# Kernel tuning notes

Hardware: AMD Instinct MI355X
Metric: run time of the kernel (lower is better)

Reference implementation:

```python
import jax, jax.numpy as jnp
import numpy as np

V, D, H, L, MAXS = 32000, 768, 12, 6, 2048
HD = D // H  # 64
FF = 4 * D
B, S = 8, 1024
EPS = 1e-5


def _make_pe():
    pos = np.arange(MAXS, dtype=np.float32)[:, None]
    div = np.exp(np.arange(0, D, 2, dtype=np.float32) * (-np.log(10000.0) / D))
    pe = np.zeros((MAXS, D), dtype=np.float32)
    pe[:, 0::2] = np.sin(pos * div)
    pe[:, 1::2] = np.cos(pos * div)
    return jnp.asarray(pe)


def setup_inputs() -> dict:
    key = jax.random.key(0)
    ks = jax.random.split(key, 16)
    sc = 0.02
    return {
        "tokens": jax.random.randint(ks[0], (B, S), 0, V),
        "k_mask": jnp.ones((B, S), dtype=jnp.int32),
        "emb": jax.random.normal(ks[1], (V, D), jnp.float32) * sc,
        "pe": _make_pe(),
        "ln1_s": jnp.ones((L, D), jnp.float32),
        "ln1_b": jnp.zeros((L, D), jnp.float32),
        "wq": jax.random.normal(ks[2], (L, H, D, HD), jnp.float32) * sc,
        "wk": jax.random.normal(ks[3], (L, H, D, HD), jnp.float32) * sc,
        "wv": jax.random.normal(ks[4], (L, H, D, HD), jnp.float32) * sc,
        "wo": jax.random.normal(ks[5], (L, D, D), jnp.float32) * sc,
        "ln2_s": jnp.ones((L, D), jnp.float32),
        "ln2_b": jnp.zeros((L, D), jnp.float32),
        "w1": jax.random.normal(ks[6], (L, D, FF), jnp.float32) * sc,
        "b1": jnp.zeros((L, FF), jnp.float32),
        "w2": jax.random.normal(ks[7], (L, FF, D), jnp.float32) * sc,
        "b2": jnp.zeros((L, D), jnp.float32),
    }


def _ln(x, s, b):
    m = jnp.mean(x, axis=-1, keepdims=True)
    v = jnp.var(x, axis=-1, keepdims=True)
    return (x - m) * jax.lax.rsqrt(v + EPS) * s + b


def _forward(tokens, k_mask, emb, pe, ln1_s, ln1_b, wq, wk, wv, wo,
             ln2_s, ln2_b, w1, b1, w2, b2):
    x = emb[tokens] + pe[None, :tokens.shape[1], :]  # [B,S,D]
    mask = (k_mask != 0)[:, None, None, :]  # [B,1,1,S]
    for l in range(L):
        xn = _ln(x, ln1_s[l], ln1_b[l])
        q = jnp.einsum('bsd,hde->bhse', xn, wq[l])
        k = jnp.einsum('bsd,hde->bhse', xn, wk[l])
        v = jnp.einsum('bsd,hde->bhse', xn, wv[l])
        scores = jnp.einsum('bhse,bhte->bhst', q, k) / (HD ** 0.5)
        scores = jnp.where(mask, scores, -jnp.inf)
        attn = jax.nn.softmax(scores, axis=-1)
        o = jnp.einsum('bhst,bhte->bhse', attn, v)  # [B,H,S,HD]
        o = o.transpose(0, 2, 1, 3).reshape(x.shape)  # concat heads -> [B,S,D]
        x = x + o @ wo[l]
        xn = _ln(x, ln2_s[l], ln2_b[l])
        h = jax.nn.gelu(xn @ w1[l] + b1[l], approximate=False)
        x = x + h @ w2[l] + b2[l]
    return x


def reference(tokens, k_mask, emb, pe, ln1_s, ln1_b, wq, wk, wv, wo,
              ln2_s, ln2_b, w1, b1, w2, b2):
    return _forward(tokens, k_mask, emb, pe, ln1_s, ln1_b, wq, wk, wv, wo,
                    ln2_s, ln2_b, w1, b1, w2, b2)
```

## Files before the change

kernel.cpp:

```cpp
#include <hip/hip_runtime.h>
#include <math.h>

typedef unsigned short u16;
typedef unsigned int u32;
typedef __attribute__((ext_vector_type(8))) __bf16 bf16x8;
typedef __attribute__((ext_vector_type(4))) float f32x4;
typedef __attribute__((ext_vector_type(8))) unsigned short ushort8v;
typedef __attribute__((ext_vector_type(4))) float float4v;
typedef __attribute__((ext_vector_type(4))) unsigned short u16x4;

typedef const __attribute__((address_space(1))) void gvoid_t;
typedef __attribute__((address_space(3))) void lvoid_t;

#define MFMA(a, b, c) __builtin_amdgcn_mfma_f32_16x16x32_bf16((a), (b), (c), 0, 0, 0)

__device__ __forceinline__ u16 f2bf(float f) {
  __bf16 h = (__bf16)f;
  return __builtin_bit_cast(u16, h);
}

__device__ __forceinline__ void stage64(const u16* g, int ldg, u16* lds, int rows, int tid) {
  int w = tid >> 6, l = tid & 63;
  int lr = l >> 3;
  int cb = (l & 7) << 4;
  for (int it = 0; it < rows; it += 32) {
    int rbase = it + w * 8;
    int r = rbase + lr;
    int scb = cb ^ ((r & 7) << 4);
    const char* gp = (const char*)(g + (size_t)r * ldg) + scb;
    char* lp = (char*)lds + (size_t)rbase * 128;
    __builtin_amdgcn_global_load_lds((gvoid_t*)gp, (lvoid_t*)lp, 16, 0, 0);
  }
}

__device__ __forceinline__ bf16x8 ldsfrag(const u16* base, int row, int e0) {
  int boff = row * 128 + (((e0) << 1) ^ ((row & 7) << 4));
  return *(const bf16x8*)((const char*)base + boff);
}

__global__ void embed_kernel(const int* __restrict__ tok, const float* __restrict__ emb,
                             const float* __restrict__ pe, float* __restrict__ xf) {
  int row = blockIdx.x;
  int tid = threadIdx.x;
  int t = tok[row];
  int spos = row & 1023;
  float4v e = ((const float4v*)(emb + (size_t)t * 768))[tid];
  float4v p = ((const float4v*)(pe + (size_t)spos * 768))[tid];
  float4v r;
  r.x = e.x + p.x; r.y = e.y + p.y; r.z = e.z + p.z; r.w = e.w + p.w;
  ((float4v*)(xf + (size_t)row * 768))[tid] = r;
}

__global__ void ln_kernel(const float* __restrict__ x, const float* __restrict__ sc,
                          const float* __restrict__ bi, u16* __restrict__ out) {
  int row = blockIdx.x;
  int tid = threadIdx.x;
  float4v v = ((const float4v*)(x + (size_t)row * 768))[tid];
  float s = v.x + v.y + v.z + v.w;
  float s2 = v.x * v.x + v.y * v.y + v.z * v.z + v.w * v.w;
  #pragma unroll
  for (int off = 32; off >= 1; off >>= 1) {
    s += __shfl_down(s, off);
    s2 += __shfl_down(s2, off);
  }
  __shared__ float red[8];
  if ((tid & 63) == 0) { red[tid >> 6] = s; red[4 + (tid >> 6)] = s2; }
  __syncthreads();
  float S = red[0] + red[1] + red[2];
  float S2 = red[4] + red[5] + red[6];
  float m = S * (1.0f / 768.0f);
  float var = S2 * (1.0f / 768.0f) - m * m;
  float rs = rsqrtf(var + 1e-5f);
  float4v sv = ((const float4v*)sc)[tid];
  float4v bv = ((const float4v*)bi)[tid];
  u16x4 ov;
  ov.x = f2bf((v.x - m) * rs * sv.x + bv.x);
  ov.y = f2bf((v.y - m) * rs * sv.y + bv.y);
  ov.z = f2bf((v.z - m) * rs * sv.z + bv.z);
  ov.w = f2bf((v.w - m) * rs * sv.w + bv.w);
  *(u16x4*)(out + (size_t)row * 768 + tid * 4) = ov;
}

__global__ void convT_kernel(const float* __restrict__ src, u16* __restrict__ dst,
                             int N, int K, long long sz, long long dz) {
  src += (size_t)blockIdx.z * sz;
  dst += (size_t)blockIdx.z * dz;
  __shared__ float t[32][33];
  int n0 = blockIdx.x * 32, k0 = blockIdx.y * 32;
  int tid = threadIdx.x;
  int tx = tid & 31, ty = tid >> 5;
  for (int r = ty; r < 32; r += 8) t[r][tx] = src[(size_t)(k0 + r) * N + n0 + tx];
  __syncthreads();
  for (int r = ty; r < 32; r += 8) dst[(size_t)(n0 + r) * K + k0 + tx] = f2bf(t[tx][r]);
}

__global__ void convqkvT_kernel(const float* __restrict__ wq, const float* __restrict__ wk,
                                const float* __restrict__ wv, u16* __restrict__ dst,
                                long long wz, long long dz) {
  __shared__ float t[32][33];
  int n0 = blockIdx.x * 32, k0 = blockIdx.y * 32;
  int which = n0 / 768;
  int r0 = n0 % 768;
  int h = r0 >> 6, e0 = r0 & 63;
  const float* src = which == 0 ? wq : (which == 1 ? wk : wv);
  src += (size_t)blockIdx.z * wz;
  dst += (size_t)blockIdx.z * dz;
  int tid = threadIdx.x;
  int tx = tid & 31, ty = tid >> 5;
  for (int r = ty; r < 32; r += 8) t[r][tx] = src[(size_t)(h * 768 + k0 + r) * 64 + e0 + tx];
  __syncthreads();
  for (int r = ty; r < 32; r += 8) dst[(size_t)(n0 + r) * 768 + k0 + tx] = f2bf(t[tx][r]);
}

__global__ void transpose_v_kernel(const u16* __restrict__ v, u16* __restrict__ vt) {
  __shared__ u16 t[64][72];
  int bh = blockIdx.x, sc = blockIdx.y;
  int tid = threadIdx.x;
  const u16* src = v + ((size_t)bh * 1024 + sc * 64) * 64;
  int sl = tid >> 2, e0 = (tid & 3) * 16;
  ushort8v a = *(const ushort8v*)(src + (size_t)sl * 64 + e0);
  ushort8v b = *(const ushort8v*)(src + (size_t)sl * 64 + e0 + 8);
  #pragma unroll
  for (int j = 0; j < 8; ++j) t[sl][e0 + j] = a[j];
  #pragma unroll
  for (int j = 0; j < 8; ++j) t[sl][e0 + 8 + j] = b[j];
  __syncthreads();
  int e = tid >> 2, s0 = (tid & 3) * 16;
  ushort8v o0, o1;
  #pragma unroll
  for (int j = 0; j < 8; ++j) o0[j] = t[s0 + j][e];
  #pragma unroll
  for (int j = 0; j < 8; ++j) o1[j] = t[s0 + 8 + j][e];
  u16* dst = vt + ((size_t)bh * 64 + e) * 1024 + sc * 64 + s0;
  *(ushort8v*)dst = o0;
  *(ushort8v*)(dst + 8) = o1;
}

template <int MODE>
__global__ __launch_bounds__(256) void gemm128(
    const u16* __restrict__ A, int lda, const u16* __restrict__ Wt, int K,
    float* __restrict__ xf, u16* __restrict__ outb, const float* __restrict__ bias,
    u16* __restrict__ qb, u16* __restrict__ kb, u16* __restrict__ vb) {
  __shared__ alignas(16) u16 As[128 * 64];
  __shared__ alignas(16) u16 Bs[128 * 64];
  int tid = threadIdx.x, lane = tid & 63, w = tid >> 6;
  int wm = w >> 1, wn = w & 1;
  int m0 = blockIdx.x * 128, n0 = blockIdx.y * 128;
  f32x4 acc[4][4] = {};
  const u16* Ag = A + (size_t)m0 * lda;
  const u16* Bg = Wt + (size_t)n0 * K;
  int arow = wm * 64 + (lane & 15);
  int brow = wn * 64 + (lane & 15);
  int e0 = (lane >> 4) * 8;
  for (int kt = 0; kt < K; kt += 64) {
    __syncthreads();
    stage64(Ag + kt, lda, As, 128, tid);
    stage64(Bg + kt, K, Bs, 128, tid);
    __syncthreads();
    #pragma unroll
    for (int kk = 0; kk < 2; ++kk) {
      bf16x8 af[4], bfr[4];
      #pragma unroll
      for (int mt = 0; mt < 4; ++mt) af[mt] = ldsfrag(As, arow + mt * 16, kk * 32 + e0);
      #pragma unroll
      for (int nt = 0; nt < 4; ++nt) bfr[nt] = ldsfrag(Bs, brow + nt * 16, kk * 32 + e0);
      #pragma unroll
      for (int mt = 0; mt < 4; ++mt)
        #pragma unroll
        for (int nt = 0; nt < 4; ++nt)
          acc[mt][nt] = MFMA(af[mt], bfr[nt], acc[mt][nt]);
    }
  }
  int rbase = m0 + wm * 64 + ((lane >> 4) << 2);
  int cbase = n0 + wn * 64 + (lane & 15);
  if constexpr (MODE == 0) {
    int which = n0 / 768;
    u16* dstb = which == 0 ? qb : (which == 1 ? kb : vb);
    int cloc = cbase - which * 768;
    #pragma unroll
    for (int mt = 0; mt < 4; ++mt) {
      #pragma unroll
      for (int nt = 0; nt < 4; ++nt) {
        int rr = cloc + nt * 16;
        int h = rr >> 6, e = rr & 63;
        #pragma unroll
        for (int reg = 0; reg < 4; ++reg) {
          int row = rbase + mt * 16 + reg;
          int b = row >> 10, s = row & 1023;
          dstb[((size_t)(b * 12 + h) * 1024 + s) * 64 + e] = f2bf(acc[mt][nt][reg]);
        }
      }
    }
  } else {
    #pragma unroll
    for (int mt = 0; mt < 4; ++mt) {
      #pragma unroll
      for (int nt = 0; nt < 4; ++nt) {
        int col = cbase + nt * 16;
        #pragma unroll
        for (int reg = 0; reg < 4; ++reg) {
          int row = rbase + mt * 16 + reg;
          float val = acc[mt][nt][reg];
          if constexpr (MODE == 1) {
            xf[(size_t)row * 768 + col] += val;
          } else if constexpr (MODE == 2) {
            float t = val + bias[col];
            float u = t * fmaf(t * t, 0.044715f, 1.0f);
            float ex = __builtin_amdgcn_exp2f(u * -2.3022156f);
            float g = t * __builtin_amdgcn_rcpf(1.0f + ex);
            outb[(size_t)row * 3072 + col] = f2bf(g);
          } else {
            xf[(size_t)row * 768 + col] += val + bias[col];
          }
        }
      }
    }
  }
}

__global__ __launch_bounds__(256) void flash64(
    const u16* __restrict__ q, const u16* __restrict__ k, const u16* __restrict__ vt,
    const int* __restrict__ kmask, u16* __restrict__ o) {
  __shared__ alignas(16) u16 Qs[64 * 64];
  __shared__ alignas(16) u16 Ks[64 * 64];
  __shared__ alignas(16) u16 Vs[64 * 64];
  __shared__ alignas(16) u16 Ps[64 * 64];
  int tid = threadIdx.x, lane = tid & 63, w = tid >> 6;
  int lc = lane & 15;
  int bh = blockIdx.x, q0 = blockIdx.y * 64;
  int b = bh / 12, h = bh % 12;

  stage64(q + ((size_t)bh * 1024 + q0) * 64, 64, Qs, 64, tid);
  __syncthreads();
  int qrow = w * 16 + lc;
  int e0 = (lane >> 4) * 8;
  bf16x8 aq0 = ldsfrag(Qs, qrow, e0);
  bf16x8 aq1 = ldsfrag(Qs, qrow, 32 + e0);

  bf16x8 ones;
  #pragma unroll
  for (int j = 0; j < 8; ++j) ones[j] = (__bf16)1.0f;

  f32x4 oacc[4] = {};
  f32x4 lacc = {};
  const float SCL = 0.125f * 1.44269504f;
  const float SH = -3.0f * 1.44269504f;
  int prow_base = w * 16 + ((lane >> 4) << 2);

  for (int kt = 0; kt < 16; ++kt) {
    __syncthreads();
    stage64(k + ((size_t)bh * 1024 + kt * 64) * 64, 64, Ks, 64, tid);
    stage64(vt + (size_t)bh * 64 * 1024 + kt * 64, 1024, Vs, 64, tid);
    __syncthreads();

    f32x4 sacc[4] = {};
    #pragma unroll
    for (int nt = 0; nt < 4; ++nt) {
      bf16x8 bk = ldsfrag(Ks, nt * 16 + lc, e0);
      sacc[nt] = MFMA(aq0, bk, sacc[nt]);
    }
    #pragma unroll
    for (int nt = 0; nt < 4; ++nt) {
      bf16x8 bk = ldsfrag(Ks, nt * 16 + lc, 32 + e0);
      sacc[nt] = MFMA(aq1, bk, sacc[nt]);
    }

    #pragma unroll
    for (int nt = 0; nt < 4; ++nt) {
      int c = nt * 16 + lc;
      float mk = kmask[b * 1024 + kt * 64 + c] ? SH : -1e30f;
      #pragma unroll
      for (int r = 0; r < 4; ++r) {
        float p = __builtin_amdgcn_exp2f(fmaf(sacc[nt][r], SCL, mk));
        int prow = prow_base + r;
        int boff = prow * 128 + ((c << 1) ^ ((prow & 7) << 4));
        *(u16*)((char*)Ps + boff) = f2bf(p);
      }
    }

    bf16x8 ap0 = ldsfrag(Ps, qrow, e0);
    bf16x8 ap1 = ldsfrag(Ps, qrow, 32 + e0);
    lacc = MFMA(ap0, ones, lacc);
    lacc = MFMA(ap1, ones, lacc);
    #pragma unroll
    for (int et = 0; et < 4; ++et) {
      bf16x8 bv = ldsfrag(Vs, et * 16 + lc, e0);
      oacc[et] = MFMA(ap0, bv, oacc[et]);
    }
    #pragma unroll
    for (int et = 0; et < 4; ++et) {
      bf16x8 bv = ldsfrag(Vs, et * 16 + lc, 32 + e0);
      oacc[et] = MFMA(ap1, bv, oacc[et]);
    }
  }

  float rl[4];
  #pragma unroll
  for (int r = 0; r < 4; ++r) rl[r] = __builtin_amdgcn_rcpf(lacc[r]);
  int orow_base = q0 + prow_base;
  #pragma unroll
  for (int et = 0; et < 4; ++et) {
    int e = et * 16 + lc;
    #pragma unroll
    for (int r = 0; r < 4; ++r) {
      int row = orow_base + r;
      o[((size_t)(b * 1024 + row)) * 768 + h * 64 + e] = f2bf(oacc[et][r] * rl[r]);
    }
  }
}

__global__ void copy_kernel(const float* __restrict__ src, float* __restrict__ dst) {
  size_t i = (size_t)blockIdx.x * blockDim.x + threadIdx.x;
  ((float4v*)dst)[i] = ((const float4v*)src)[i];
}

extern "C" void kernel_launch(void* const* d_in, const int* in_sizes, int n_in,
                              void* d_out, int out_size, void* d_ws, size_t ws_size,
                              hipStream_t stream) {
  const int* tokens = (const int*)d_in[0];
  const int* kmask = (const int*)d_in[1];
  const float* emb = (const float*)d_in[2];
  const float* pe = (const float*)d_in[3];
  const float* ln1_s = (const float*)d_in[4];
  const float* ln1_b = (const float*)d_in[5];
  const float* wq = (const float*)d_in[6];
  const float* wk = (const float*)d_in[7];
  const float* wv = (const float*)d_in[8];
  const float* wo = (const float*)d_in[9];
  const float* ln2_s = (const float*)d_in[10];
  const float* ln2_b = (const float*)d_in[11];
  const float* w1 = (const float*)d_in[12];
  const float* b1 = (const float*)d_in[13];
  const float* w2 = (const float*)d_in[14];
  const float* b2 = (const float*)d_in[15];

  char* ws = (char*)d_ws;
  float* xf = (float*)ws;
  u16* xn   = (u16*)(ws + 25165824);
  u16* qb   = (u16*)(ws + 37748736);
  u16* kb   = (u16*)(ws + 50331648);
  u16* vb   = (u16*)(ws + 62914560);
  u16* vtb  = (u16*)(ws + 75497472);
  u16* ob   = (u16*)(ws + 88080384);
  u16* ffh  = (u16*)(ws + 100663296);

  const size_t SZ_QKV = (size_t)2304 * 768;
  const size_t SZ_O   = (size_t)768 * 768;
  const size_t SZ_F1  = (size_t)3072 * 768;
  const size_t SZ_F2  = (size_t)768 * 3072;
  const size_t NEED = 150994944 + 2 * 6 * (SZ_QKV + SZ_O + SZ_F1 + SZ_F2);
  bool pre = ws_size >= NEED;
  int nz = pre ? 6 : 1;
  u16* wqkvt = (u16*)(ws + 150994944);
  u16* wot   = wqkvt + (size_t)nz * SZ_QKV;
  u16* w1t   = wot + (size_t)nz * SZ_O;
  u16* w2t   = w1t + (size_t)nz * SZ_F1;

  embed_kernel<<<8192, 192, 0, stream>>>(tokens, emb, pe, xf);

  if (pre) {
    convqkvT_kernel<<<dim3(72, 24, 6), 256, 0, stream>>>(wq, wk, wv, wqkvt, 589824LL, (long long)SZ_QKV);
    convT_kernel<<<dim3(24, 24, 6), 256, 0, stream>>>(wo, wot, 768, 768, 589824LL, (long long)SZ_O);
    convT_kernel<<<dim3(96, 24, 6), 256, 0, stream>>>(w1, w1t, 3072, 768, 2359296LL, (long long)SZ_F1);
    convT_kernel<<<dim3(24, 96, 6), 256, 0, stream>>>(w2, w2t, 768, 3072, 2359296LL, (long long)SZ_F2);
  }

  for (int l = 0; l < 6; ++l) {
    size_t woff_qkv = (size_t)l * 12 * 768 * 64;
    size_t woff_o = (size_t)l * 768 * 768;
    size_t woff_ff = (size_t)l * 768 * 3072;
    const u16* wt_qkv_l = wqkvt + (pre ? (size_t)l * SZ_QKV : 0);
    const u16* wt_o_l   = wot   + (pre ? (size_t)l * SZ_O   : 0);
    const u16* wt_1_l   = w1t   + (pre ? (size_t)l * SZ_F1  : 0);
    const u16* wt_2_l   = w2t   + (pre ? (size_t)l * SZ_F2  : 0);

    if (!pre) {
      convqkvT_kernel<<<dim3(72, 24, 1), 256, 0, stream>>>(wq + woff_qkv, wk + woff_qkv, wv + woff_qkv, (u16*)wt_qkv_l, 0LL, 0LL);
      convT_kernel<<<dim3(24, 24, 1), 256, 0, stream>>>(wo + woff_o, (u16*)wt_o_l, 768, 768, 0LL, 0LL);
      convT_kernel<<<dim3(96, 24, 1), 256, 0, stream>>>(w1 + woff_ff, (u16*)wt_1_l, 3072, 768, 0LL, 0LL);
      convT_kernel<<<dim3(24, 96, 1), 256, 0, stream>>>(w2 + woff_ff, (u16*)wt_2_l, 768, 3072, 0LL, 0LL);
    }

    ln_kernel<<<8192, 192, 0, stream>>>(xf, ln1_s + l * 768, ln1_b + l * 768, xn);
    gemm128<0><<<dim3(64, 18), 256, 0, stream>>>(xn, 768, wt_qkv_l, 768, nullptr, nullptr, nullptr, qb, kb, vb);
    transpose_v_kernel<<<dim3(96, 16), 256, 0, stream>>>(vb, vtb);
    flash64<<<dim3(96, 16), 256, 0, stream>>>(qb, kb, vtb, kmask, ob);
    gemm128<1><<<dim3(64, 6), 256, 0, stream>>>(ob, 768, wt_o_l, 768, xf, nullptr, nullptr, nullptr, nullptr, nullptr);
    ln_kernel<<<8192, 192, 0, stream>>>(xf, ln2_s + l * 768, ln2_b + l * 768, xn);
    gemm128<2><<<dim3(64, 24), 256, 0, stream>>>(xn, 768, wt_1_l, 768, nullptr, ffh, b1 + l * 3072, nullptr, nullptr, nullptr);
    gemm128<3><<<dim3(64, 6), 256, 0, stream>>>(ffh, 3072, wt_2_l, 3072, xf, nullptr, b2 + l * 768, nullptr, nullptr, nullptr);
  }

  copy_kernel<<<6144, 256, 0, stream>>>(xf, (float*)d_out);
}
```

Baseline: 1.686 ms.

## Use direct global-to-LDS loads, split-K with atomics, and double-buffer flash K/V

```diff
diff --git a/kernel.cpp b/kernel.cpp
--- a/kernel.cpp
+++ b/kernel.cpp
@@ -136,9 +136,9 @@
   *(ushort8v*)(dst + 8) = o1;
 }
 
-template <int MODE>
+template <int MODE, int NK>
 __global__ __launch_bounds__(256) void gemm128(
-    const u16* __restrict__ A, int lda, const u16* __restrict__ Wt, int K,
+    const u16* __restrict__ A, int lda, const u16* __restrict__ Wt, int ldb,
     float* __restrict__ xf, u16* __restrict__ outb, const float* __restrict__ bias,
     u16* __restrict__ qb, u16* __restrict__ kb, u16* __restrict__ vb) {
   __shared__ alignas(16) u16 As[128 * 64];
@@ -146,16 +146,29 @@
   int tid = threadIdx.x, lane = tid & 63, w = tid >> 6;
   int wm = w >> 1, wn = w & 1;
   int m0 = blockIdx.x * 128, n0 = blockIdx.y * 128;
+  int kb0 = blockIdx.z * (NK * 64);
   f32x4 acc[4][4] = {};
-  const u16* Ag = A + (size_t)m0 * lda;
-  const u16* Bg = Wt + (size_t)n0 * K;
+  int lr = lane >> 3;
+  int cb = (lane & 7) << 4;
+  int sws = cb ^ (lr << 4);
+  const char* pA = (const char*)(A + (size_t)m0 * lda + kb0) + (size_t)(w * 8 + lr) * (lda * 2) + sws;
+  const char* pB = (const char*)(Wt + (size_t)n0 * ldb + kb0) + (size_t)(w * 8 + lr) * (ldb * 2) + sws;
+  char* dA = (char*)As + w * 1024;
+  char* dB = (char*)Bs + w * 1024;
   int arow = wm * 64 + (lane & 15);
   int brow = wn * 64 + (lane & 15);
   int e0 = (lane >> 4) * 8;
-  for (int kt = 0; kt < K; kt += 64) {
+  #pragma unroll
+  for (int kt = 0; kt < NK; ++kt) {
     __syncthreads();
-    stage64(Ag + kt, lda, As, 128, tid);
-    stage64(Bg + kt, K, Bs, 128, tid);
+    #pragma unroll
+    for (int i = 0; i < 4; ++i) {
+      __builtin_amdgcn_global_load_lds((gvoid_t*)(pA + (size_t)i * 32 * (lda * 2)),
+                                       (lvoid_t*)(dA + i * 4096), 16, 0, 0);
+      __builtin_amdgcn_global_load_lds((gvoid_t*)(pB + (size_t)i * 32 * (ldb * 2)),
+                                       (lvoid_t*)(dB + i * 4096), 16, 0, 0);
+    }
+    pA += 128; pB += 128;
     __syncthreads();
     #pragma unroll
     for (int kk = 0; kk < 2; ++kk) {
@@ -191,27 +204,36 @@
         }
       }
     }
-  } else {
+  } else if constexpr (MODE == 2) {
     #pragma unroll
     for (int mt = 0; mt < 4; ++mt) {
       #pragma unroll
       for (int nt = 0; nt < 4; ++nt) {
         int col = cbase + nt * 16;
+        float bb = bias[col];
         #pragma unroll
         for (int reg = 0; reg < 4; ++reg) {
           int row = rbase + mt * 16 + reg;
-          float val = acc[mt][nt][reg];
-          if constexpr (MODE == 1) {
-            xf[(size_t)row * 768 + col] += val;
-          } else if constexpr (MODE == 2) {
-            float t = val + bias[col];
-            float u = t * fmaf(t * t, 0.044715f, 1.0f);
-            float ex = __builtin_amdgcn_exp2f(u * -2.3022156f);
-            float g = t * __builtin_amdgcn_rcpf(1.0f + ex);
-            outb[(size_t)row * 3072 + col] = f2bf(g);
-          } else {
-            xf[(size_t)row * 768 + col] += val + bias[col];
-          }
+          float t = acc[mt][nt][reg] + bb;
+          float u = t * fmaf(t * t, 0.044715f, 1.0f);
+          float ex = __builtin_amdgcn_exp2f(u * -2.3022156f);
+          float g = t * __builtin_amdgcn_rcpf(1.0f + ex);
+          outb[(size_t)row * 3072 + col] = f2bf(g);
+        }
+      }
+    }
+  } else {
+    bool addb = (MODE == 3) && (blockIdx.z == 0);
+    #pragma unroll
+    for (int mt = 0; mt < 4; ++mt) {
+      #pragma unroll
+      for (int nt = 0; nt < 4; ++nt) {
+        int col = cbase + nt * 16;
+        float bb = addb ? bias[col] : 0.0f;
+        #pragma unroll
+        for (int reg = 0; reg < 4; ++reg) {
+          int row = rbase + mt * 16 + reg;
+          atomicAdd(&xf[(size_t)row * 768 + col], acc[mt][nt][reg] + bb);
         }
       }
     }
@@ -222,8 +244,8 @@
     const u16* __restrict__ q, const u16* __restrict__ k, const u16* __restrict__ vt,
     const int* __restrict__ kmask, u16* __restrict__ o) {
   __shared__ alignas(16) u16 Qs[64 * 64];
-  __shared__ alignas(16) u16 Ks[64 * 64];
-  __shared__ alignas(16) u16 Vs[64 * 64];
+  __shared__ alignas(16) u16 Ks[2][64 * 64];
+  __shared__ alignas(16) u16 Vs[2][64 * 64];
   __shared__ alignas(16) u16 Ps[64 * 64];
   int tid = threadIdx.x, lane = tid & 63, w = tid >> 6;
   int lc = lane & 15;
@@ -247,22 +269,32 @@
   const float SH = -3.0f * 1.44269504f;
   int prow_base = w * 16 + ((lane >> 4) << 2);
 
+  stage64(k + (size_t)bh * 1024 * 64, 64, Ks[0], 64, tid);
+  stage64(vt + (size_t)bh * 64 * 1024, 1024, Vs[0], 64, tid);
+
   for (int kt = 0; kt < 16; ++kt) {
-    __syncthreads();
-    stage64(k + ((size_t)bh * 1024 + kt * 64) * 64, 64, Ks, 64, tid);
-    stage64(vt + (size_t)bh * 64 * 1024 + kt * 64, 1024, Vs, 64, tid);
-    __syncthreads();
+    asm volatile("s_waitcnt vmcnt(0)" ::: "memory");
+    __builtin_amdgcn_sched_barrier(0);
+    __builtin_amdgcn_s_barrier();
+    __builtin_amdgcn_sched_barrier(0);
+    const u16* Kc = Ks[kt & 1];
+    const u16* Vc = Vs[kt & 1];
 
     f32x4 sacc[4] = {};
     #pragma unroll
     for (int nt = 0; nt < 4; ++nt) {
-      bf16x8 bk = ldsfrag(Ks, nt * 16 + lc, e0);
+      bf16x8 bk = ldsfrag(Kc, nt * 16 + lc, e0);
       sacc[nt] = MFMA(aq0, bk, sacc[nt]);
     }
     #pragma unroll
     for (int nt = 0; nt < 4; ++nt) {
-      bf16x8 bk = ldsfrag(Ks, nt * 16 + lc, 32 + e0);
+      bf16x8 bk = ldsfrag(Kc, nt * 16 + lc, 32 + e0);
       sacc[nt] = MFMA(aq1, bk, sacc[nt]);
+    }
+
+    if (kt + 1 < 16) {
+      stage64(k + ((size_t)bh * 1024 + (kt + 1) * 64) * 64, 64, Ks[(kt + 1) & 1], 64, tid);
+      stage64(vt + (size_t)bh * 64 * 1024 + (kt + 1) * 64, 1024, Vs[(kt + 1) & 1], 64, tid);
     }
 
     #pragma unroll
@@ -284,12 +316,12 @@
     lacc = MFMA(ap1, ones, lacc);
     #pragma unroll
     for (int et = 0; et < 4; ++et) {
-      bf16x8 bv = ldsfrag(Vs, et * 16 + lc, e0);
+      bf16x8 bv = ldsfrag(Vc, et * 16 + lc, e0);
       oacc[et] = MFMA(ap0, bv, oacc[et]);
     }
     #pragma unroll
     for (int et = 0; et < 4; ++et) {
-      bf16x8 bv = ldsfrag(Vs, et * 16 + lc, 32 + e0);
+      bf16x8 bv = ldsfrag(Vc, et * 16 + lc, 32 + e0);
       oacc[et] = MFMA(ap1, bv, oacc[et]);
     }
   }
@@ -382,13 +414,13 @@
     }
 
     ln_kernel<<<8192, 192, 0, stream>>>(xf, ln1_s + l * 768, ln1_b + l * 768, xn);
-    gemm128<0><<<dim3(64, 18), 256, 0, stream>>>(xn, 768, wt_qkv_l, 768, nullptr, nullptr, nullptr, qb, kb, vb);
+    gemm128<0, 12><<<dim3(64, 18, 1), 256, 0, stream>>>(xn, 768, wt_qkv_l, 768, nullptr, nullptr, nullptr, qb, kb, vb);
     transpose_v_kernel<<<dim3(96, 16), 256, 0, stream>>>(vb, vtb);
     flash64<<<dim3(96, 16), 256, 0, stream>>>(qb, kb, vtb, kmask, ob);
-    gemm128<1><<<dim3(64, 6), 256, 0, stream>>>(ob, 768, wt_o_l, 768, xf, nullptr, nullptr, nullptr, nullptr, nullptr);
+    gemm128<1, 6><<<dim3(64, 6, 2), 256, 0, stream>>>(ob, 768, wt_o_l, 768, xf, nullptr, nullptr, nullptr, nullptr, nullptr);
     ln_kernel<<<8192, 192, 0, stream>>>(xf, ln2_s + l * 768, ln2_b + l * 768, xn);
-    gemm128<2><<<dim3(64, 24), 256, 0, stream>>>(xn, 768, wt_1_l, 768, nullptr, ffh, b1 + l * 3072, nullptr, nullptr, nullptr);
-    gemm128<3><<<dim3(64, 6), 256, 0, stream>>>(ffh, 3072, wt_2_l, 3072, xf, nullptr, b2 + l * 768, nullptr, nullptr, nullptr);
+    gemm128<2, 12><<<dim3(64, 24, 1), 256, 0, stream>>>(xn, 768, wt_1_l, 768, nullptr, ffh, b1 + l * 3072, nullptr, nullptr, nullptr);
+    gemm128<3, 16><<<dim3(64, 6, 3), 256, 0, stream>>>(ffh, 3072, wt_2_l, 3072, xf, nullptr, b2 + l * 768, nullptr, nullptr, nullptr);
   }
 
   copy_kernel<<<6144, 256, 0, stream>>>(xf, (float*)d_out);
```

After: 1.830 ms. +8.5%, slower.
